# Kernel tuning notes

Measured on AMD Instinct MI355X. Metric: run time of the kernel, lower is better.

## Reference

```python
import jax, jax.numpy as jnp
import numpy as np

N_NODES = 100000

def graph_conv(x, src, dst, W_rel, W_root, b, num_nodes):
    # PyG GraphConv: out_i = lin_rel(sum_{j in N(i)} x_j) + lin_root(x_i)
    agg = jax.ops.segment_sum(x[src], dst, num_segments=num_nodes)  # [N, F_in]
    return agg @ W_rel + x @ W_root + b


def setup_inputs() -> dict:
    key = jax.random.key(0)
    ks = jax.random.split(key, 8)
    z = jax.random.normal(ks[0], (N_NODES, 64), dtype=jnp.float32)
    edge_index = jax.random.randint(ks[1], (2, 1600000), 0, N_NODES, dtype=jnp.int64)
    def glorot(k, fi, fo):
        s = (6.0 / (fi + fo)) ** 0.5
        return jax.random.uniform(k, (fi, fo), dtype=jnp.float32, minval=-s, maxval=s)
    return {
        "z": z,
        "edge_index": edge_index,
        "W_rel1": glorot(ks[2], 64, 32), "W_root1": glorot(ks[3], 64, 32), "b1": jnp.zeros((32,), jnp.float32),
        "W_rel2": glorot(ks[4], 32, 16), "W_root2": glorot(ks[5], 32, 16), "b2": jnp.zeros((16,), jnp.float32),
        "W_rel3": glorot(ks[6], 16, 2), "W_root3": glorot(ks[7], 16, 2), "b3": jnp.zeros((2,), jnp.float32),
    }


def reference(z, edge_index, W_rel1, W_root1, b1, W_rel2, W_root2, b2, W_rel3, W_root3, b3):
    src, dst = edge_index[0], edge_index[1]
    h = graph_conv(z, src, dst, W_rel1, W_root1, b1, N_NODES)
    h = jax.nn.relu(h)
    h = graph_conv(h, src, dst, W_rel2, W_root2, b2, N_NODES)
    h = jax.nn.relu(h)
    h = graph_conv(h, src, dst, W_rel3, W_root3, b3, N_NODES)
    return jax.nn.softmax(h, axis=-1)
```

## Files before the change

kernel.cpp:

```cpp
#include <hip/hip_runtime.h>
#include <hip/hip_bf16.h>


#define RNODES 128
#define NB_MAX 1024
#define CH 4096
#define CMAX 512

template <int Fin, int Fout, bool RELU>
__global__ void linear2_kernel(const float* __restrict__ x,
                               const float* __restrict__ Wrel,
                               const float* __restrict__ Wroot,
                               const float* __restrict__ bias,
                               float* __restrict__ t,
                               float* __restrict__ acc, int N) {
    const bool rootTask = (blockIdx.y != 0);
    const float* __restrict__ W = rootTask ? Wroot : Wrel;
    float* __restrict__ outp    = rootTask ? acc : t;

    int n = blockIdx.x * blockDim.x + threadIdx.x;
    if (n >= N) return;

    float o[Fout];
#pragma unroll
    for (int f = 0; f < Fout; ++f) o[f] = 0.f;

    const float* xr = x + (size_t)n * Fin;
    for (int k0 = 0; k0 < Fin; k0 += 16) {
#pragma unroll
        for (int k = 0; k < 16; k += 4) {
            float4 v = *(const float4*)(xr + k0 + k);
            if (RELU) {
                v.x = fmaxf(v.x, 0.f); v.y = fmaxf(v.y, 0.f);
                v.z = fmaxf(v.z, 0.f); v.w = fmaxf(v.w, 0.f);
            }
            const float xv[4] = {v.x, v.y, v.z, v.w};
#pragma unroll
            for (int kk = 0; kk < 4; ++kk) {
                const float* wr = W + (size_t)(k0 + k + kk) * Fout;
#pragma unroll
                for (int f = 0; f < Fout; ++f)
                    o[f] = fmaf(xv[kk], wr[f], o[f]);
            }
        }
    }
    if (rootTask) {
#pragma unroll
        for (int f = 0; f < Fout; ++f) o[f] += bias[f];
    }
    float* op = outp + (size_t)n * Fout;
    if constexpr (Fout >= 4) {
#pragma unroll
        for (int f = 0; f < Fout; f += 4)
            *(float4*)(op + f) = make_float4(o[f], o[f + 1], o[f + 2], o[f + 3]);
    } else {
        *(float2*)op = make_float2(o[0], o[1]);
    }
}

__global__ void hist_chunked_kernel(const int* __restrict__ dst,
                                    int* __restrict__ chunkhist,
                                    int nE, int NB) {
    __shared__ int h[NB_MAX];
    const int c  = blockIdx.x;
    const int e0 = c * CH, e1 = min(e0 + CH, nE);
    for (int b = threadIdx.x; b < NB; b += blockDim.x) h[b] = 0;
    __syncthreads();
    for (int e = e0 + threadIdx.x; e < e1; e += blockDim.x)
        atomicAdd(&h[dst[e] >> 7], 1);
    __syncthreads();
    for (int b = threadIdx.x; b < NB; b += blockDim.x)
        chunkhist[(size_t)c * NB + b] = h[b];
}

__global__ void scan_chunkhist_kernel(int* __restrict__ chunkhist,
                                      int* __restrict__ gtotal,
                                      int C, int NB) {
    __shared__ int s[CMAX];
    const int b = blockIdx.x;
    const int t = threadIdx.x;
    int v = (t < C) ? chunkhist[(size_t)t * NB + b] : 0;
    s[t] = v;
    __syncthreads();
    for (int off = 1; off < CMAX; off <<= 1) {
        int u = (t >= off) ? s[t - off] : 0;
        __syncthreads();
        s[t] += u;
        __syncthreads();
    }
    if (t < C) chunkhist[(size_t)t * NB + b] = s[t] - v;
    if (t == CMAX - 1) gtotal[b] = s[t];
}

__global__ void scan_buckets_kernel(const int* __restrict__ gtotal,
                                    int* __restrict__ bptr, int NB, int nE) {
    __shared__ int s[NB_MAX];
    int t = threadIdx.x;
    int own = (t < NB) ? gtotal[t] : 0;
    s[t] = own;
    __syncthreads();
    for (int off = 1; off < NB_MAX; off <<= 1) {
        int v = (t >= off) ? s[t - off] : 0;
        __syncthreads();
        s[t] += v;
        __syncthreads();
    }
    if (t < NB) bptr[t] = s[t] - own;
    if (t == 0) bptr[NB] = nE;
}

__global__ void bucketize_det_kernel(const int* __restrict__ src,
                                     const int* __restrict__ dst,
                                     const int* __restrict__ chunkpre,
                                     const int* __restrict__ bptr,
                                     unsigned int* __restrict__ records,
                                     int nE, int NB) {
    __shared__ int lcur[NB_MAX];
    const int c  = blockIdx.x;
    const int e0 = c * CH, e1 = min(e0 + CH, nE);
    for (int b = threadIdx.x; b < NB; b += blockDim.x)
        lcur[b] = bptr[b] + chunkpre[(size_t)c * NB + b];
    __syncthreads();
    for (int e = e0 + threadIdx.x; e < e1; e += blockDim.x) {
        int d = dst[e];
        int b = d >> 7;
        int pos = atomicAdd(&lcur[b], 1);
        records[pos] = (unsigned int)src[e] | ((unsigned int)(d & 127) << 17);
    }
}

__global__ void place_merge_kernel(const unsigned int* __restrict__ records,
                                   const int* __restrict__ bptr,
                                   int* __restrict__ rowptr,
                                   int* __restrict__ srcs_sorted,
                                   int N, int nE, int NB) {
    __shared__ int hist[RNODES];
    __shared__ int s[RNODES];
    __shared__ int lcur[RNODES];
    const int b    = blockIdx.x;
    const int base = b * RNODES;
    const int nn   = min(RNODES, N - base);
    const int beg  = bptr[b], end = bptr[b + 1];
    const int t    = threadIdx.x;

    if (t < RNODES) hist[t] = 0;
    __syncthreads();
    for (int i = beg + t; i < end; i += blockDim.x)
        atomicAdd(&hist[records[i] >> 17], 1);
    __syncthreads();

    if (t < RNODES) s[t] = hist[t];
    __syncthreads();
    for (int off = 1; off < RNODES; off <<= 1) {
        int v = (t < RNODES && t >= off) ? s[t - off] : 0;
        __syncthreads();
        if (t < RNODES && t >= off) s[t] += v;
        __syncthreads();
    }
    if (t < nn) {
        int ex = beg + s[t] - hist[t];
        rowptr[base + t] = ex;
        lcur[t] = ex;
    }
    if (b == NB - 1 && t == 0) rowptr[N] = nE;
    __syncthreads();

    for (int i = beg + t; i < end; i += blockDim.x) {
        unsigned int rec = records[i];
        int pos = atomicAdd(&lcur[rec >> 17], 1);
        srcs_sorted[pos] = (int)(rec & 0x1FFFFu);
    }
}

template <int F, bool SOFTMAX>
__global__ void gather_agg_kernel(const float* __restrict__ t,
                                  const int* __restrict__ rowptr,
                                  const int* __restrict__ srcs,
                                  const float* __restrict__ rootacc,
                                  float* __restrict__ out, int N) {
    int tid = blockIdx.x * blockDim.x + threadIdx.x;
    int n = tid / F;
    if (n >= N) return;
    int f = tid & (F - 1);
    const float* tf = t + f;
    int beg = rowptr[n], end = rowptr[n + 1];
    float sum = 0.0f;
    int e = beg;
    for (; e + 16 <= end; e += 16) {
        int s[16];
        float v[16];
#pragma unroll
        for (int u = 0; u < 16; ++u) s[u] = srcs[e + u];
#pragma unroll
        for (int u = 0; u < 16; ++u) v[u] = tf[(long)s[u] * F];
#pragma unroll
        for (int u = 0; u < 16; ++u) sum += v[u];
    }
    for (; e + 4 <= end; e += 4) {
        int s[4];
        float v[4];
#pragma unroll
        for (int u = 0; u < 4; ++u) s[u] = srcs[e + u];
#pragma unroll
        for (int u = 0; u < 4; ++u) v[u] = tf[(long)s[u] * F];
        sum += (v[0] + v[1]) + (v[2] + v[3]);
    }
    for (; e < end; ++e) sum += tf[(long)srcs[e] * F];

    float v = rootacc[(long)n * F + f] + sum;
    if (!SOFTMAX) {
        out[(long)n * F + f] = v;
    } else {
        float o = __shfl_xor(v, 1, 64);
        float m = fmaxf(v, o);
        float ev = __expf(v - m), eo = __expf(o - m);
        out[(long)n * F + f] = ev / (ev + eo);
    }
}

template <int F>
__global__ void scatter_kernel(const float* __restrict__ t,
                               const int* __restrict__ src,
                               const int* __restrict__ dst,
                               float* __restrict__ acc, int nE) {
    int tid = blockIdx.x * blockDim.x + threadIdx.x;
    int e = tid / F;
    if (e >= nE) return;
    int f = tid & (F - 1);
    atomicAdd(acc + (long)dst[e] * F + f, t[(long)src[e] * F + f]);
}

__global__ void softmax2_kernel(const float* __restrict__ h, float* __restrict__ out, int N) {
    int n = blockIdx.x * blockDim.x + threadIdx.x;
    if (n >= N) return;
    float a = h[2 * n], b = h[2 * n + 1];
    float m = fmaxf(a, b);
    float ea = __expf(a - m), eb = __expf(b - m);
    float inv = 1.0f / (ea + eb);
    out[2 * n] = ea * inv;
    out[2 * n + 1] = eb * inv;
}

extern "C" void kernel_launch(void* const* d_in, const int* in_sizes, int n_in,
                              void* d_out, int out_size, void* d_ws, size_t ws_size,
                              hipStream_t stream) {
    const float* z      = (const float*)d_in[0];
    const int*   ei     = (const int*)d_in[1];
    const float* Wrel1  = (const float*)d_in[2];
    const float* Wroot1 = (const float*)d_in[3];
    const float* b1     = (const float*)d_in[4];
    const float* Wrel2  = (const float*)d_in[5];
    const float* Wroot2 = (const float*)d_in[6];
    const float* b2     = (const float*)d_in[7];
    const float* Wrel3  = (const float*)d_in[8];
    const float* Wroot3 = (const float*)d_in[9];
    const float* b3     = (const float*)d_in[10];

    const int N  = in_sizes[0] / 64;
    const int nE = in_sizes[1] / 2;
    const int* src = ei;
    const int* dst = ei + nE;
    const int NB = (N + RNODES - 1) / RNODES;
    const int C  = (nE + CH - 1) / CH;

    float* regionA = (float*)d_ws;
    float* regionB = regionA + (size_t)N * 32;
    float* t1 = regionA;
    float* h1 = regionB;
    float* t2 = regionA;
    float* h2 = regionA + (size_t)N * 16;
    float* t3 = regionB;
    float* h3 = regionB + (size_t)N * 2;
    unsigned int* records = (unsigned int*)regionA;

    int* chunkhist = (int*)regionB;
    int* gtotal    = chunkhist + (size_t)CMAX * NB_MAX;
    int* bptr      = gtotal + NB_MAX;
    int* ibase       = (int*)(regionB + (size_t)N * 32);
    int* rowptr      = ibase;
    int* srcs_sorted = rowptr + N + 1;

    size_t needed = (size_t)N * 64 * sizeof(float)
                  + ((size_t)N + 1 + (size_t)nE) * sizeof(int);
    size_t buildNeed = ((size_t)CMAX * NB_MAX + NB_MAX + NB_MAX + 1) * sizeof(int);

    const int B = 256;
    const int nodeBlocks = (N + B - 1) / B;
    const dim3 linGrid(nodeBlocks, 2);
    const bool packOK = (N <= (1 << 17)) && (NB <= NB_MAX) && (C <= CMAX)
                      && ((size_t)nE * 4 <= (size_t)N * 32 * 4)
                      && (buildNeed <= (size_t)N * 32 * 4);

    if (ws_size >= needed && packOK) {
        hist_chunked_kernel<<<C, 512, 0, stream>>>(dst, chunkhist, nE, NB);
        scan_chunkhist_kernel<<<NB, CMAX, 0, stream>>>(chunkhist, gtotal, C, NB);
        scan_buckets_kernel<<<1, NB_MAX, 0, stream>>>(gtotal, bptr, NB, nE);
        bucketize_det_kernel<<<C, 512, 0, stream>>>(src, dst, chunkhist, bptr, records, nE, NB);
        place_merge_kernel<<<NB, 512, 0, stream>>>(records, bptr, rowptr, srcs_sorted, N, nE, NB);

        linear2_kernel<64, 32, false><<<linGrid, B, 0, stream>>>(z, Wrel1, Wroot1, b1, t1, h1, N);
        gather_agg_kernel<32, false><<<((size_t)N * 32 + B - 1) / B, B, 0, stream>>>(
            t1, rowptr, srcs_sorted, h1, h1, N);

        linear2_kernel<32, 16, true><<<linGrid, B, 0, stream>>>(h1, Wrel2, Wroot2, b2, t2, h2, N);
        gather_agg_kernel<16, false><<<((size_t)N * 16 + B - 1) / B, B, 0, stream>>>(
            t2, rowptr, srcs_sorted, h2, h2, N);

        linear2_kernel<16, 2, true><<<linGrid, B, 0, stream>>>(h2, Wrel3, Wroot3, b3, t3, h3, N);
        gather_agg_kernel<2, true><<<((size_t)N * 2 + B - 1) / B, B, 0, stream>>>(
            t3, rowptr, srcs_sorted, h3, (float*)d_out, N);
    } else {
        linear2_kernel<64, 32, false><<<linGrid, B, 0, stream>>>(z, Wrel1, Wroot1, b1, t1, h1, N);
        scatter_kernel<32><<<((size_t)nE * 32 + B - 1) / B, B, 0, stream>>>(t1, src, dst, h1, nE);
        linear2_kernel<32, 16, true><<<linGrid, B, 0, stream>>>(h1, Wrel2, Wroot2, b2, t2, h2, N);
        scatter_kernel<16><<<((size_t)nE * 16 + B - 1) / B, B, 0, stream>>>(t2, src, dst, h2, nE);
        linear2_kernel<16, 2, true><<<linGrid, B, 0, stream>>>(h2, Wrel3, Wroot3, b3, t3, h3, N);
        scatter_kernel<2><<<((size_t)nE * 2 + B - 1) / B, B, 0, stream>>>(t3, src, dst, h3, nE);
        softmax2_kernel<<<nodeBlocks, B, 0, stream>>>(h3, (float*)d_out, N);
    }
}
```

Baseline: 248.4 us.

## Quantize gathered features to int16 with per-node scale, fuse rel/root linears

The transformed neighbour features are now stored as int16 with a per-node scale, which halves the bytes each gather has to fetch. Each gather thread now handles two features packed into one int. The rel and root linear transforms are fused into a single kernel that reads x only once. The workspace is reorganised into separate aligned buffers, and the full unroll of the linear k-loop raises register pressure. The change adds quantization error (about 15-bit relative to each row's max) and one extra scale load per edge.

```diff
diff --git a/kernel.cpp b/kernel.cpp
--- a/kernel.cpp
+++ b/kernel.cpp
@@ -1,11 +1,77 @@
 #include <hip/hip_runtime.h>
-#include <hip/hip_bf16.h>
 
 
 #define RNODES 128
 #define NB_MAX 1024
 #define CH 4096
 #define CMAX 512
+
+template <int Fin, int Fout, bool RELU>
+__global__ void linear_fused_q_kernel(const float* __restrict__ x,
+                                      const float* __restrict__ Wrel,
+                                      const float* __restrict__ Wroot,
+                                      const float* __restrict__ bias,
+                                      short* __restrict__ t,
+                                      float* __restrict__ tscale,
+                                      float* __restrict__ acc, int N) {
+    int n = blockIdx.x * blockDim.x + threadIdx.x;
+    if (n >= N) return;
+
+    float orel[Fout], oroot[Fout];
+#pragma unroll
+    for (int f = 0; f < Fout; ++f) { orel[f] = 0.f; oroot[f] = 0.f; }
+
+    const float* xr = x + (size_t)n * Fin;
+#pragma unroll
+    for (int k = 0; k < Fin; k += 4) {
+        float4 v = *(const float4*)(xr + k);
+        if (RELU) {
+            v.x = fmaxf(v.x, 0.f); v.y = fmaxf(v.y, 0.f);
+            v.z = fmaxf(v.z, 0.f); v.w = fmaxf(v.w, 0.f);
+        }
+        const float xv[4] = {v.x, v.y, v.z, v.w};
+#pragma unroll
+        for (int kk = 0; kk < 4; ++kk) {
+            const float* wr1 = Wrel  + (size_t)(k + kk) * Fout;
+            const float* wr2 = Wroot + (size_t)(k + kk) * Fout;
+#pragma unroll
+            for (int f = 0; f < Fout; ++f) {
+                orel[f]  = fmaf(xv[kk], wr1[f], orel[f]);
+                oroot[f] = fmaf(xv[kk], wr2[f], oroot[f]);
+            }
+        }
+    }
+
+    float m = 0.f;
+#pragma unroll
+    for (int f = 0; f < Fout; ++f) m = fmaxf(m, fabsf(orel[f]));
+    const float inv = (m > 0.f) ? (32767.0f / m) : 0.f;
+    tscale[n] = m * (1.0f / 32767.0f);
+
+    short q[Fout];
+#pragma unroll
+    for (int f = 0; f < Fout; ++f) q[f] = (short)__float2int_rn(orel[f] * inv);
+
+    short* trow = t + (size_t)n * Fout;
+    if constexpr (Fout >= 8) {
+#pragma unroll
+        for (int f = 0; f < Fout; f += 8)
+            *(int4*)(trow + f) = *(const int4*)(q + f);
+    } else {
+        *(int*)trow = (int)(unsigned short)q[0] | ((int)q[1] << 16);
+    }
+
+#pragma unroll
+    for (int f = 0; f < Fout; ++f) oroot[f] += bias[f];
+    float* arow = acc + (size_t)n * Fout;
+    if constexpr (Fout >= 4) {
+#pragma unroll
+        for (int f = 0; f < Fout; f += 4)
+            *(float4*)(arow + f) = make_float4(oroot[f], oroot[f+1], oroot[f+2], oroot[f+3]);
+    } else {
+        *(float2*)arow = make_float2(oroot[0], oroot[1]);
+    }
+}
 
 template <int Fin, int Fout, bool RELU>
 __global__ void linear2_kernel(const float* __restrict__ x,
@@ -26,22 +92,20 @@
     for (int f = 0; f < Fout; ++f) o[f] = 0.f;
 
     const float* xr = x + (size_t)n * Fin;
-    for (int k0 = 0; k0 < Fin; k0 += 16) {
-#pragma unroll
-        for (int k = 0; k < 16; k += 4) {
-            float4 v = *(const float4*)(xr + k0 + k);
-            if (RELU) {
-                v.x = fmaxf(v.x, 0.f); v.y = fmaxf(v.y, 0.f);
-                v.z = fmaxf(v.z, 0.f); v.w = fmaxf(v.w, 0.f);
-            }
-            const float xv[4] = {v.x, v.y, v.z, v.w};
-#pragma unroll
-            for (int kk = 0; kk < 4; ++kk) {
-                const float* wr = W + (size_t)(k0 + k + kk) * Fout;
-#pragma unroll
-                for (int f = 0; f < Fout; ++f)
-                    o[f] = fmaf(xv[kk], wr[f], o[f]);
-            }
+#pragma unroll
+    for (int k = 0; k < Fin; k += 4) {
+        float4 v = *(const float4*)(xr + k);
+        if (RELU) {
+            v.x = fmaxf(v.x, 0.f); v.y = fmaxf(v.y, 0.f);
+            v.z = fmaxf(v.z, 0.f); v.w = fmaxf(v.w, 0.f);
+        }
+        const float xv[4] = {v.x, v.y, v.z, v.w};
+#pragma unroll
+        for (int kk = 0; kk < 4; ++kk) {
+            const float* wr = W + (size_t)(k + kk) * Fout;
+#pragma unroll
+            for (int f = 0; f < Fout; ++f)
+                o[f] = fmaf(xv[kk], wr[f], o[f]);
         }
     }
     if (rootTask) {
@@ -173,48 +237,58 @@
 }
 
 template <int F, bool SOFTMAX>
-__global__ void gather_agg_kernel(const float* __restrict__ t,
-                                  const int* __restrict__ rowptr,
-                                  const int* __restrict__ srcs,
-                                  const float* __restrict__ rootacc,
-                                  float* __restrict__ out, int N) {
+__global__ void gather_agg_q_kernel(const short* __restrict__ t,
+                                    const float* __restrict__ tscale,
+                                    const int* __restrict__ rowptr,
+                                    const int* __restrict__ srcs,
+                                    const float* __restrict__ rootacc,
+                                    float* __restrict__ out, int N) {
+    constexpr int P = (F >= 4) ? (F / 2) : 1;
+    constexpr int S = F / 2;
     int tid = blockIdx.x * blockDim.x + threadIdx.x;
-    int n = tid / F;
+    int n  = (P == 1) ? tid : (tid / P);
+    int fp = (P == 1) ? 0   : (tid & (P - 1));
     if (n >= N) return;
-    int f = tid & (F - 1);
-    const float* tf = t + f;
+
+    const int* tp = (const int*)t;
     int beg = rowptr[n], end = rowptr[n + 1];
-    float sum = 0.0f;
+    float sx = 0.f, sy = 0.f;
     int e = beg;
-    for (; e + 16 <= end; e += 16) {
-        int s[16];
-        float v[16];
-#pragma unroll
-        for (int u = 0; u < 16; ++u) s[u] = srcs[e + u];
-#pragma unroll
-        for (int u = 0; u < 16; ++u) v[u] = tf[(long)s[u] * F];
-#pragma unroll
-        for (int u = 0; u < 16; ++u) sum += v[u];
-    }
-    for (; e + 4 <= end; e += 4) {
-        int s[4];
-        float v[4];
-#pragma unroll
-        for (int u = 0; u < 4; ++u) s[u] = srcs[e + u];
-#pragma unroll
-        for (int u = 0; u < 4; ++u) v[u] = tf[(long)s[u] * F];
-        sum += (v[0] + v[1]) + (v[2] + v[3]);
-    }
-    for (; e < end; ++e) sum += tf[(long)srcs[e] * F];
-
-    float v = rootacc[(long)n * F + f] + sum;
+    for (; e + 8 <= end; e += 8) {
+        int s[8];
+#pragma unroll
+        for (int u = 0; u < 8; ++u) s[u] = srcs[e + u];
+        int q[8]; float sc[8];
+#pragma unroll
+        for (int u = 0; u < 8; ++u) {
+            q[u]  = tp[s[u] * S + fp];
+            sc[u] = tscale[s[u]];
+        }
+#pragma unroll
+        for (int u = 0; u < 8; ++u) {
+            float lo = (float)((short)(q[u] & 0xFFFF));
+            float hi = (float)(q[u] >> 16);
+            sx = fmaf(sc[u], lo, sx);
+            sy = fmaf(sc[u], hi, sy);
+        }
+    }
+    for (; e < end; ++e) {
+        int s0 = srcs[e];
+        int qv = tp[s0 * S + fp];
+        float sc = tscale[s0];
+        sx = fmaf(sc, (float)((short)(qv & 0xFFFF)), sx);
+        sy = fmaf(sc, (float)(qv >> 16), sy);
+    }
+
+    const float2 r0 = *(const float2*)(rootacc + (size_t)n * F + 2 * fp);
+    float a = r0.x + sx, b = r0.y + sy;
     if (!SOFTMAX) {
-        out[(long)n * F + f] = v;
+        *(float2*)(out + (size_t)n * F + 2 * fp) = make_float2(a, b);
     } else {
-        float o = __shfl_xor(v, 1, 64);
-        float m = fmaxf(v, o);
-        float ev = __expf(v - m), eo = __expf(o - m);
-        out[(long)n * F + f] = ev / (ev + eo);
+        float m = fmaxf(a, b);
+        float ea = __expf(a - m), eb = __expf(b - m);
+        float inv = 1.0f / (ea + eb);
+        *(float2*)(out + (size_t)n * 2) = make_float2(ea * inv, eb * inv);
     }
 }
 
@@ -263,33 +337,33 @@
     const int NB = (N + RNODES - 1) / RNODES;
     const int C  = (nE + CH - 1) / CH;
 
-    float* regionA = (float*)d_ws;
-    float* regionB = regionA + (size_t)N * 32;
-    float* t1 = regionA;
-    float* h1 = regionB;
-    float* t2 = regionA;
-    float* h2 = regionA + (size_t)N * 16;
-    float* t3 = regionB;
-    float* h3 = regionB + (size_t)N * 2;
-    unsigned int* records = (unsigned int*)regionA;
-
-    int* chunkhist = (int*)regionB;
-    int* gtotal    = chunkhist + (size_t)CMAX * NB_MAX;
-    int* bptr      = gtotal + NB_MAX;
-    int* ibase       = (int*)(regionB + (size_t)N * 32);
-    int* rowptr      = ibase;
-    int* srcs_sorted = rowptr + N + 1;
-
-    size_t needed = (size_t)N * 64 * sizeof(float)
-                  + ((size_t)N + 1 + (size_t)nE) * sizeof(int);
-    size_t buildNeed = ((size_t)CMAX * NB_MAX + NB_MAX + NB_MAX + 1) * sizeof(int);
+    char* wsb = (char*)d_ws;
+    size_t off = 0;
+    auto take = [&](size_t bytes) -> void* {
+        void* p = (void*)(wsb + off);
+        off = (off + bytes + 255) & ~(size_t)255;
+        return p;
+    };
+    int*          chunkhist   = (int*)take((size_t)CMAX * NB_MAX * 4);
+    int*          gtotal      = (int*)take((size_t)NB_MAX * 4);
+    int*          bptr        = (int*)take((size_t)(NB_MAX + 1) * 4);
+    unsigned int* records     = (unsigned int*)take((size_t)nE * 4);
+    int*          rowptr      = (int*)take((size_t)(N + 1) * 4);
+    int*          srcs_sorted = (int*)take((size_t)nE * 4);
+    short*        t1          = (short*)take((size_t)N * 32 * 2);
+    float*        s1          = (float*)take((size_t)N * 4);
+    float*        h1          = (float*)take((size_t)N * 32 * 4);
+    short*        t2          = (short*)take((size_t)N * 16 * 2);
+    float*        s2          = (float*)take((size_t)N * 4);
+    float*        h2          = (float*)take((size_t)N * 16 * 4);
+    short*        t3          = (short*)take((size_t)N * 2 * 2);
+    float*        s3          = (float*)take((size_t)N * 4);
+    float*        h3          = (float*)take((size_t)N * 2 * 4);
+    const size_t needed = off;
 
     const int B = 256;
     const int nodeBlocks = (N + B - 1) / B;
-    const dim3 linGrid(nodeBlocks, 2);
-    const bool packOK = (N <= (1 << 17)) && (NB <= NB_MAX) && (C <= CMAX)
-                      && ((size_t)nE * 4 <= (size_t)N * 32 * 4)
-                      && (buildNeed <= (size_t)N * 32 * 4);
+    const bool packOK = (N <= (1 << 17)) && (NB <= NB_MAX) && (C <= CMAX);
 
     if (ws_size >= needed && packOK) {
         hist_chunked_kernel<<<C, 512, 0, stream>>>(dst, chunkhist, nE, NB);
@@ -298,24 +372,36 @@
         bucketize_det_kernel<<<C, 512, 0, stream>>>(src, dst, chunkhist, bptr, records, nE, NB);
         place_merge_kernel<<<NB, 512, 0, stream>>>(records, bptr, rowptr, srcs_sorted, N, nE, NB);
 
-        linear2_kernel<64, 32, false><<<linGrid, B, 0, stream>>>(z, Wrel1, Wroot1, b1, t1, h1, N);
-        gather_agg_kernel<32, false><<<((size_t)N * 32 + B - 1) / B, B, 0, stream>>>(
-            t1, rowptr, srcs_sorted, h1, h1, N);
-
-        linear2_kernel<32, 16, true><<<linGrid, B, 0, stream>>>(h1, Wrel2, Wroot2, b2, t2, h2, N);
-        gather_agg_kernel<16, false><<<((size_t)N * 16 + B - 1) / B, B, 0, stream>>>(
-            t2, rowptr, srcs_sorted, h2, h2, N);
-
-        linear2_kernel<16, 2, true><<<linGrid, B, 0, stream>>>(h2, Wrel3, Wroot3, b3, t3, h3, N);
-        gather_agg_kernel<2, true><<<((size_t)N * 2 + B - 1) / B, B, 0, stream>>>(
-            t3, rowptr, srcs_sorted, h3, (float*)d_out, N);
+        linear_fused_q_kernel<64, 32, false><<<nodeBlocks, B, 0, stream>>>(
+            z, Wrel1, Wroot1, b1, t1, s1, h1, N);
+        gather_agg_q_kernel<32, false><<<((size_t)N * 16 + B - 1) / B, B, 0, stream>>>(
+            t1, s1, rowptr, srcs_sorted, h1, h1, N);
+
+        linear_fused_q_kernel<32, 16, true><<<nodeBlocks, B, 0, stream>>>(
+            h1, Wrel2, Wroot2, b2, t2, s2, h2, N);
+        gather_agg_q_kernel<16, false><<<((size_t)N * 8 + B - 1) / B, B, 0, stream>>>(
+            t2, s2, rowptr, srcs_sorted, h2, h2, N);
+
+        linear_fused_q_kernel<16, 2, true><<<nodeBlocks, B, 0, stream>>>(
+            h2, Wrel3, Wroot3, b3, t3, s3, h3, N);
+        gather_agg_q_kernel<2, true><<<((size_t)N + B - 1) / B, B, 0, stream>>>(
+            t3, s3, rowptr, srcs_sorted, h3, (float*)d_out, N);
     } else {
-        linear2_kernel<64, 32, false><<<linGrid, B, 0, stream>>>(z, Wrel1, Wroot1, b1, t1, h1, N);
-        scatter_kernel<32><<<((size_t)nE * 32 + B - 1) / B, B, 0, stream>>>(t1, src, dst, h1, nE);
-        linear2_kernel<32, 16, true><<<linGrid, B, 0, stream>>>(h1, Wrel2, Wroot2, b2, t2, h2, N);
-        scatter_kernel<16><<<((size_t)nE * 16 + B - 1) / B, B, 0, stream>>>(t2, src, dst, h2, nE);
-        linear2_kernel<16, 2, true><<<linGrid, B, 0, stream>>>(h2, Wrel3, Wroot3, b3, t3, h3, N);
-        scatter_kernel<2><<<((size_t)nE * 2 + B - 1) / B, B, 0, stream>>>(t3, src, dst, h3, nE);
-        softmax2_kernel<<<nodeBlocks, B, 0, stream>>>(h3, (float*)d_out, N);
-    }
-}
+        float* regionA = (float*)d_ws;
+        float* regionB = regionA + (size_t)N * 32;
+        float* ft1 = regionA;
+        float* fh1 = regionB;
+        float* ft2 = regionA;
+        float* fh2 = regionA + (size_t)N * 16;
+        float* ft3 = regionB;
+        float* fh3 = regionB + (size_t)N * 2;
+        const dim3 linGrid(nodeBlocks, 2);
+        linear2_kernel<64, 32, false><<<linGrid, B, 0, stream>>>(z, Wrel1, Wroot1, b1, ft1, fh1, N);
+        scatter_kernel<32><<<((size_t)nE * 32 + B - 1) / B, B, 0, stream>>>(ft1, src, dst, fh1, nE);
+        linear2_kernel<32, 16, true><<<linGrid, B, 0, stream>>>(fh1, Wrel2, Wroot2, b2, ft2, fh2, N);
+        scatter_kernel<16><<<((size_t)nE * 16 + B - 1) / B, B, 0, stream>>>(ft2, src, dst, fh2, nE);
+        linear2_kernel<16, 2, true><<<linGrid, B, 0, stream>>>(fh2, Wrel3, Wroot3, b3, ft3, fh3, N);
+        scatter_kernel<2><<<((size_t)nE * 2 + B - 1) / B, B, 0, stream>>>(ft3, src, dst, fh3, nE);
+        softmax2_kernel<<<nodeBlocks, B, 0, stream>>>(fh3, (float*)d_out, N);
+    }
+}
```

Measured after the change: 266.4 us. +7.3%, slower.
